# Optimization experiments

Hardware: AMD Instinct MI355X
Metric: run time of the kernel (lower is better)

## Reference

```python
import jax, jax.numpy as jnp
import numpy as np

K = 3           # kernel_size
PAD = 1         # padding
HEADS = 6
C = 192
CH = C // HEADS           # channels per head = 32
SCALE = CH ** (-0.5)
KK = K * K                # 9


def unfold3(x):
    # x: [N,C,H,W] -> [N,C,9,H,W] (im2col with k=3, pad=1, stride=1)
    N, c, H, W = x.shape
    xp = jnp.pad(x, ((0, 0), (0, 0), (PAD, PAD), (PAD, PAD)))
    return jnp.stack([xp[:, :, i:i + H, j:j + W] for i in range(K) for j in range(K)], axis=2)


def fold3(y):
    # y: [N,C,9,H,W] -> [N,C,H,W] (scatter-add inverse of unfold3)
    N, c, kk, H, W = y.shape
    out = jnp.zeros((N, c, H + 2 * PAD, W + 2 * PAD), dtype=y.dtype)
    idx = 0
    for i in range(K):
        for j in range(K):
            out = out.at[:, :, i:i + H, j:j + W].add(y[:, :, idx])
            idx += 1
    return out[:, :, PAD:PAD + H, PAD:PAD + W]


def setup_inputs() -> dict:
    key = jax.random.key(0)
    ks = jax.random.split(key, 6)
    N, H, W = 16, 56, 56
    s = 0.02
    return {
        "x": jax.random.normal(ks[0], (N, C, H, W), jnp.float32),
        "Wv": jax.random.normal(ks[1], (C, C), jnp.float32) * s,          # fc (no bias)
        "Wa": jax.random.normal(ks[2], (C, KK * KK * HEADS), jnp.float32) * s,  # fc_att weight
        "ba": jax.random.normal(ks[3], (KK * KK * HEADS,), jnp.float32) * s,
        "Wp": jax.random.normal(ks[4], (C, C), jnp.float32) * s,          # fc_proj weight
        "bp": jax.random.normal(ks[5], (C,), jnp.float32) * s,
    }


def reference(x, Wv, Wa, ba, Wp, bp):
    N, c, H, W = x.shape
    HW = H * W
    # value projection (pointwise linear over channels)
    v = jnp.einsum("nchw,cd->ndhw", x, Wv)
    # unfold values: [N,C,9,H,W] -> [N,heads,ch,9,HW] -> [N,heads,HW,9,ch]
    vu = unfold3(v).reshape(N, HEADS, CH, KK, HW).transpose(0, 1, 4, 3, 2)
    # attention logits from (avg-pooled, here identity since stride=1) input
    att = jnp.einsum("nchw,ck->nhwk", x, Wa) + ba       # [N,H,W,81*heads]
    att = att.reshape(N, HW, HEADS, KK, KK).transpose(0, 2, 1, 3, 4)  # [N,heads,HW,9,9]
    att = jax.nn.softmax(att * SCALE, axis=-1)          # dropout is identity at inference
    # apply per-position 9x9 attention to the 9 gathered neighbors
    out = jnp.einsum("nhpkl,nhplc->nhpkc", att, vu)      # [N,heads,HW,9,ch]
    # fold back: layout (heads, ch, kk) matches unfold layout (C, kk)
    out = out.transpose(0, 1, 4, 3, 2).reshape(N, c, KK, H, W)
    folded = fold3(out)                                  # [N,C,H,W]
    # output projection
    return jnp.einsum("nchw,cd->ndhw", folded, Wp) + bp[None, :, None, None]
```

## Files before the change

### kernel.cpp

```cpp
#include <hip/hip_runtime.h>
#include <hip/hip_bf16.h>
#include <math.h>

#define HW 3136
#define NPOS 50176
#define NC 192
#define NHEADS 6
#define IMG 56
#define NATT 486
#define ATT_SCALE 0.17677669529663687f

typedef __attribute__((ext_vector_type(8))) short short8;
typedef __attribute__((ext_vector_type(8))) unsigned short ushort8;
typedef __attribute__((ext_vector_type(4))) float float4v;
typedef __attribute__((ext_vector_type(4))) unsigned int uint4v;

__device__ __forceinline__ float bf2f(unsigned short u) {
    unsigned int x = ((unsigned int)u) << 16;
    return __builtin_bit_cast(float, x);
}
__device__ __forceinline__ float bf2f_lo(unsigned int u) {
    return __builtin_bit_cast(float, u << 16);
}
__device__ __forceinline__ float bf2f_hi(unsigned int u) {
    return __builtin_bit_cast(float, u & 0xffff0000u);
}
__device__ __forceinline__ unsigned short f2bf(float f) {
    __hip_bfloat16 h = __float2bfloat16(f);
    return __builtin_bit_cast(unsigned short, h);
}
__device__ __forceinline__ void gload_lds16(const void* g, void* l) {
    __builtin_amdgcn_global_load_lds((const __attribute__((address_space(1))) void*)g,
                                     (__attribute__((address_space(3))) void*)l, 16, 0, 0);
}

__global__ __launch_bounds__(256) void transpose_x(const float* __restrict__ x,
                                                   unsigned short* __restrict__ xt)
{
    __shared__ float tile[64][65];
    int bx = blockIdx.x;
    int n = (bx * 64) / HW;
    int hw0 = (bx * 64) % HW;
    int c0 = blockIdx.y * 64;
    int tl = threadIdx.x & 63, tg = threadIdx.x >> 6;
    const float* xn = x + (size_t)n * NC * HW;
#pragma unroll
    for (int i = 0; i < 16; ++i)
        tile[tg * 16 + i][tl] = xn[(size_t)(c0 + tg * 16 + i) * HW + hw0 + tl];
    __syncthreads();
    unsigned short* xp = xt + ((size_t)n * HW + hw0) * NC + c0;
#pragma unroll
    for (int i = 0; i < 16; ++i) {
        int hwr = tg * 16 + i;
        xp[(size_t)hwr * NC + tl] = f2bf(tile[tl][hwr]);
    }
}

__global__ __launch_bounds__(256) void prep_weights(
    const float* __restrict__ Wv, const float* __restrict__ Wa, const float* __restrict__ Wp,
    const float* __restrict__ ba,
    unsigned short* __restrict__ Wall, unsigned short* __restrict__ Wpt,
    float* __restrict__ ball)
{
    int idx = blockIdx.x * 256 + threadIdx.x;
    if (idx < 36864) {
        int d = idx / 192, k = idx - d * 192;
        Wpt[idx] = f2bf(Wp[(size_t)k * NC + d]);
    }
    if (idx < 147456) {
        int d = idx / 192, k = idx - d * 192;
        unsigned short val;
        float bv = 0.f;
        if (d < 192) {
            val = f2bf(Wv[(size_t)k * NC + d]);
        } else {
            int dp = d - 192;
            int head = dp / 96, rr = dp - head * 96;
            int k9 = rr / 10, l = rr - k9 * 10;
            bool valid = (k9 < 9) && (l < 9);
            int src = head * 81 + k9 * 9 + l;
            val = valid ? f2bf(Wa[(size_t)k * NATT + src]) : (unsigned short)0;
            bv = valid ? ba[src] : 0.f;
        }
        Wall[idx] = val;
        if (k == 0) ball[d] = bv;
    }
}

__global__ __launch_bounds__(512, 4) void gemm_big(
    const unsigned short* __restrict__ A, const unsigned short* __restrict__ W,
    const float* __restrict__ ball,
    unsigned short* __restrict__ Vo, unsigned short* __restrict__ ATo)
{
    __shared__ __align__(16) unsigned short As[3][4096];
    __shared__ __align__(16) unsigned short Bs[3][4096];
    int t = threadIdx.x, lane = t & 63, wave = t >> 6;
    int bi = blockIdx.x;
    int slot = bi >> 3;
    int q6 = slot / 6;
    int rr_ = (bi & 7) + 8 * q6;
    int cc_ = slot - 6 * q6;
    int col0 = cc_ * 128, row0 = rr_ * 128;
    int fr = lane & 15, fq = lane >> 4;
    int wm = (wave >> 2) * 64, wn = (wave & 3) * 32;
    int srow = lane >> 2;
    int sg = ((lane & 3) ^ ((lane >> 3) & 3)) * 16;
    int rc = (fq ^ ((fr >> 1) & 3)) * 16;
    const char* Ab = (const char*)A;
    const char* Wb = (const char*)W;

    float4v acc[4][2] = {};

#define STAGE_BIG(buf, k0)                                                         \
    {                                                                              \
        gload_lds16(Ab + (size_t)(row0 + wave * 16 + srow) * 384 + (k0) * 2 + sg,  \
                    (char*)As[buf] + wave * 1024);                                 \
        gload_lds16(Wb + (size_t)(col0 + wave * 16 + srow) * 384 + (k0) * 2 + sg,  \
                    (char*)Bs[buf] + wave * 1024);                                 \
    }

    STAGE_BIG(0, 0);
    STAGE_BIG(1, 32);
#pragma unroll
    for (int s = 0; s < 6; ++s) {
        int buf = s % 3;
        if (s < 4) {
            STAGE_BIG((s + 2) % 3, (s + 2) * 32);
            asm volatile("s_waitcnt vmcnt(4)\n\ts_barrier" ::: "memory");
        } else if (s == 4) {
            asm volatile("s_waitcnt vmcnt(2)\n\ts_barrier" ::: "memory");
        } else {
            asm volatile("s_waitcnt vmcnt(0)\n\ts_barrier" ::: "memory");
        }
        short8 af[4], bf[2];
#pragma unroll
        for (int mi = 0; mi < 4; ++mi)
            af[mi] = *(const short8*)((const char*)As[buf] + (wm + mi * 16 + fr) * 64 + rc);
#pragma unroll
        for (int ni = 0; ni < 2; ++ni)
            bf[ni] = *(const short8*)((const char*)Bs[buf] + (wn + ni * 16 + fr) * 64 + rc);
        asm volatile("s_waitcnt lgkmcnt(0)\n\ts_barrier" ::: "memory");
#pragma unroll
        for (int mi = 0; mi < 4; ++mi)
#pragma unroll
            for (int ni = 0; ni < 2; ++ni)
                acc[mi][ni] = __builtin_amdgcn_mfma_f32_16x16x32_bf16(
                    af[mi], bf[ni], acc[mi][ni], 0, 0, 0);
    }

#pragma unroll
    for (int ni = 0; ni < 2; ++ni) {
        int col = col0 + wn + ni * 16 + fr;
        float b = ball[col];
        unsigned short* bptr;
        size_t rstr;
        bool valid;
        if (col < 192) {
            int hd = col >> 5, ch = col & 31;
            bptr = Vo + ((size_t)hd * NPOS) * 32 + ch;
            rstr = 32;
            valid = true;
        } else {
            int dp = col - 192;
            int hd = dp / 96, rr = dp - hd * 96;
            int k9 = rr / 10, l = rr - k9 * 10;
            valid = (k9 < 9);
            bptr = ATo + ((size_t)(hd * 9 + (k9 < 9 ? k9 : 8)) * NPOS) * 10 + l;
            rstr = 10;
        }
#pragma unroll
        for (int mi = 0; mi < 4; ++mi) {
            int row = row0 + wm + mi * 16 + fq * 4;
#pragma unroll
            for (int r = 0; r < 4; ++r) {
                unsigned short val = f2bf(acc[mi][ni][r] + b);
                if (valid) bptr[(size_t)(row + r) * rstr] = val;
            }
        }
    }
#undef STAGE_BIG
}

__global__ __launch_bounds__(256) void gemm_small(
    const unsigned short* __restrict__ A,
    const unsigned short* __restrict__ B,
    const float* __restrict__ bias, float* __restrict__ out)
{
    __shared__ __align__(16) unsigned short As[2][2048];
    __shared__ __align__(16) unsigned short Bs[2][8192];
    int t = threadIdx.x, lane = t & 63, wave = t >> 6;
    int n0 = blockIdx.x * 256, m0 = blockIdx.y * 64;
    int fr = lane & 15, fq = lane >> 4;
    int srow = lane >> 2;
    int sg = ((lane & 3) ^ ((lane >> 3) & 3)) * 16;
    int rc = (fq ^ ((fr >> 1) & 3)) * 16;
    const char* Ab = (const char*)A;
    const char* Bb = (const char*)B;

    float4v acc[4][4] = {};

#define STAGE_SMALL(buf, k0)                                                      \
    {                                                                             \
        gload_lds16(Ab + (size_t)(m0 + wave * 16 + srow) * 384 + (k0)*2 + sg,     \
                    (char*)As[buf] + wave * 1024);                                \
        _Pragma("unroll")                                                         \
        for (int i = 0; i < 4; ++i) {                                             \
            int j = wave * 4 + i;                                                 \
            gload_lds16(Bb + (size_t)(n0 + j * 16 + srow) * 384 + (k0)*2 + sg,    \
                        (char*)Bs[buf] + j * 1024);                               \
        }                                                                         \
    }

    STAGE_SMALL(0, 0);
    for (int s = 0; s < 6; ++s) {
        if (s < 5) {
            STAGE_SMALL((s + 1) & 1, (s + 1) * 32);
            asm volatile("s_waitcnt vmcnt(5)\n\ts_barrier" ::: "memory");
        } else {
            asm volatile("s_waitcnt vmcnt(0)\n\ts_barrier" ::: "memory");
        }
        int buf = s & 1;
        short8 af[4], bf[4];
#pragma unroll
        for (int mi = 0; mi < 4; ++mi)
            af[mi] = *(const short8*)((const char*)As[buf] + (mi * 16 + fr) * 64 + rc);
#pragma unroll
        for (int ni = 0; ni < 4; ++ni)
            bf[ni] = *(const short8*)((const char*)Bs[buf] + (wave * 64 + ni * 16 + fr) * 64 + rc);
        asm volatile("s_waitcnt lgkmcnt(0)\n\ts_barrier" ::: "memory");
#pragma unroll
        for (int mi = 0; mi < 4; ++mi)
#pragma unroll
            for (int ni = 0; ni < 4; ++ni)
                acc[mi][ni] = __builtin_amdgcn_mfma_f32_16x16x32_bf16(
                    af[mi], bf[ni], acc[mi][ni], 0, 0, 0);
    }

#pragma unroll
    for (int ni = 0; ni < 4; ++ni) {
        int n = n0 + wave * 64 + ni * 16 + fr;
        int img = n / HW, phw = n - img * HW;
        float* op = out + (size_t)img * (NC * HW) + phw;
#pragma unroll
        for (int mi = 0; mi < 4; ++mi) {
            int m = m0 + mi * 16 + fq * 4;
#pragma unroll
            for (int r = 0; r < 4; ++r)
                op[(size_t)(m + r) * HW] = acc[mi][ni][r] + bias[m + r];
        }
    }
#undef STAGE_SMALL
}

__global__ __launch_bounds__(256, 4) void fused_att_agg(
    const unsigned short* __restrict__ V, const unsigned short* __restrict__ AT,
    unsigned short* __restrict__ fold)
{
    __shared__ __align__(16) char vt[4 * 434 * 16];
    int t = threadIdx.x;
    int bid = blockIdx.x;
    int head = bid % NHEADS; int tmp = bid / NHEADS;
    int tcol = tmp & 1; tmp >>= 1;
    int trow = tmp % 7; int img = tmp / 7;
    int h0 = trow * 8, w0 = tcol * 28;

    const unsigned short* Vh = V + (size_t)head * NPOS * 32;
    ushort8 stg[6];
#pragma unroll
    for (int i = 0; i < 6; ++i) {
        int u = i * 256 + t;
        int slot = u >> 2, q = u & 3;
        int vrow = slot >> 5, vcol = slot & 31;
        int hh = h0 - 2 + vrow, ww = w0 - 2 + vcol;
        bool ok = (hh >= 0) & (hh < IMG) & (ww >= 0) & (ww < IMG);
        int hc = min(max(hh, 0), IMG - 1);
        int wcl = min(max(ww, 0), IMG - 1);
        ushort8 val = *(const ushort8*)(Vh + (size_t)(img * HW + hc * IMG + wcl) * 32 + q * 8);
        if (!ok) val = (ushort8){};
        stg[i] = val;
    }

    int ph = t / 28, pw = t - (t / 28) * 28;
    int h = h0 + ph, w = w0 + pw;
    float wc[25];
#pragma unroll
    for (int d = 0; d < 25; ++d) wc[d] = 0.f;
    if (t < 224) {
        int head9 = head * 9;
#pragma unroll
        for (int k = 0; k < 9; ++k) {
            const int oky = k / 3 - 1, okx = k % 3 - 1;
            int hh = h - oky, ww = w - okx;
            bool ok = (hh >= 0) & (hh < IMG) & (ww >= 0) & (ww < IMG);
            int hc = min(max(hh, 0), IMG - 1);
            int wcl = min(max(ww, 0), IMG - 1);
            size_t nidx = (size_t)img * HW + hc * IMG + wcl;
            const unsigned int* ap32 =
                (const unsigned int*)(AT + ((size_t)(head9 + k) * NPOS + nidx) * 10);
            unsigned int u0 = ap32[0], u1 = ap32[1], u2 = ap32[2], u3 = ap32[3], u4 = ap32[4];
            float a[9] = { bf2f_lo(u0), bf2f_hi(u0), bf2f_lo(u1), bf2f_hi(u1),
                           bf2f_lo(u2), bf2f_hi(u2), bf2f_lo(u3), bf2f_hi(u3),
                           bf2f_lo(u4) };
            float m = -1e30f;
#pragma unroll
            for (int l = 0; l < 9; ++l) m = fmaxf(m, a[l]);
            float s = 0.f;
#pragma unroll
            for (int l = 0; l < 9; ++l) {
                a[l] = __expf((a[l] - m) * ATT_SCALE);
                s += a[l];
            }
            float g = ok ? (1.f / s) : 0.f;
#pragma unroll
            for (int l = 0; l < 9; ++l) {
                const int dy = (l / 3 - 1) - oky + 2;
                const int dx = (l % 3 - 1) - okx + 2;
                wc[dy * 5 + dx] += a[l] * g;
            }
        }
    }

#pragma unroll
    for (int i = 0; i < 6; ++i) {
        int u = i * 256 + t;
        int slot = u >> 2, q = u & 3;
        int vrow = slot >> 5, vcol = slot & 31;
        *(ushort8*)(vt + q * (434 * 16) + (vrow * 36 + vcol) * 16) = stg[i];
    }
    __syncthreads();

    if (t < 224) {
        int base = (ph * 36 + pw) * 16;
        int pos = img * HW + h * IMG + w;
        unsigned short* fo = fold + (size_t)pos * NC + head * 32;
#pragma unroll
        for (int q = 0; q < 4; ++q) {
            const char* vq = vt + q * (434 * 16) + base;
            float acc[8];
#pragma unroll
            for (int j = 0; j < 8; ++j) acc[j] = 0.f;
#pragma unroll
            for (int d = 0; d < 25; ++d) {
                const int dy = d / 5, dx = d % 5;
                float wf = wc[d];
                uint4v vv = *(const uint4v*)(vq + (dy * 36 + dx) * 16);
#pragma unroll
                for (int z = 0; z < 4; ++z) {
                    acc[2 * z]     += wf * bf2f_lo(vv[z]);
                    acc[2 * z + 1] += wf * bf2f_hi(vv[z]);
                }
            }
            ushort8 ov;
#pragma unroll
            for (int j = 0; j < 8; ++j) ov[j] = f2bf(acc[j]);
            *(ushort8*)(fo + q * 8) = ov;
        }
    }
}

extern "C" void kernel_launch(void* const* d_in, const int* in_sizes, int n_in,
                              void* d_out, int out_size, void* d_ws, size_t ws_size,
                              hipStream_t stream)
{
    const float* x  = (const float*)d_in[0];
    const float* Wv = (const float*)d_in[1];
    const float* Wa = (const float*)d_in[2];
    const float* ba = (const float*)d_in[3];
    const float* Wp = (const float*)d_in[4];
    const float* bp = (const float*)d_in[5];
    float* out = (float*)d_out;

    unsigned short* xt   = (unsigned short*)d_ws;
    unsigned short* V    = xt + 9633792;
    unsigned short* AT   = V + 9633792;
    unsigned short* Wall = AT + 27095040;
    unsigned short* Wpt  = Wall + 147456;
    float*          ball = (float*)(Wpt + 36864);
    unsigned short* foldb = xt;

    dim3 blk(256);
    prep_weights<<<576, blk, 0, stream>>>(Wv, Wa, Wp, ba, Wall, Wpt, ball);
    transpose_x<<<dim3(784, 3), blk, 0, stream>>>(x, xt);
    gemm_big<<<2352, dim3(512), 0, stream>>>(xt, Wall, ball, V, AT);
    fused_att_agg<<<1344, blk, 0, stream>>>(V, AT, foldb);
    gemm_small<<<dim3(196, 3), blk, 0, stream>>>(Wpt, foldb, bp, out);
}
```

Measured before the change: 182.9 us.

## Vectorize gemm_big epilogue stores, retile gemm_small, hoist attention loads

gemm_big swaps its MFMA operands so each lane holds four consecutive output columns, which lets the epilogue write packed bf16 pairs (8-byte and 4-byte stores) instead of scattered 2-byte stores, with special cases for the 10-wide attention rows. gemm_small moves to 128-column tiles on a 1D grid with a grouped tile order, halving LDS use and adding a 4-blocks-per-CU launch bound to raise occupancy. fused_att_agg issues all attention-logit loads into registers before the LDS staging and barrier, then runs the softmax afterwards, so load latency overlaps with the staging. The packed attention stores depend on tricky column-alignment logic, and holding the raw logits across the barrier raises register pressure.

```diff
diff --git a/kernel.cpp b/kernel.cpp
--- a/kernel.cpp
+++ b/kernel.cpp
@@ -14,6 +14,7 @@
 typedef __attribute__((ext_vector_type(8))) unsigned short ushort8;
 typedef __attribute__((ext_vector_type(4))) float float4v;
 typedef __attribute__((ext_vector_type(4))) unsigned int uint4v;
+typedef __attribute__((ext_vector_type(2))) unsigned int uint2v;
 
 __device__ __forceinline__ float bf2f(unsigned short u) {
     unsigned int x = ((unsigned int)u) << 16;
@@ -28,6 +29,9 @@
 __device__ __forceinline__ unsigned short f2bf(float f) {
     __hip_bfloat16 h = __float2bfloat16(f);
     return __builtin_bit_cast(unsigned short, h);
+}
+__device__ __forceinline__ unsigned int pack2bf(float a, float b) {
+    return (unsigned int)f2bf(a) | ((unsigned int)f2bf(b) << 16);
 }
 __device__ __forceinline__ void gload_lds16(const void* g, void* l) {
     __builtin_amdgcn_global_load_lds((const __attribute__((address_space(1))) void*)g,
@@ -145,51 +149,71 @@
 #pragma unroll
             for (int ni = 0; ni < 2; ++ni)
                 acc[mi][ni] = __builtin_amdgcn_mfma_f32_16x16x32_bf16(
-                    af[mi], bf[ni], acc[mi][ni], 0, 0, 0);
+                    bf[ni], af[mi], acc[mi][ni], 0, 0, 0);
     }
 
 #pragma unroll
     for (int ni = 0; ni < 2; ++ni) {
-        int col = col0 + wn + ni * 16 + fr;
-        float b = ball[col];
-        unsigned short* bptr;
-        size_t rstr;
-        bool valid;
-        if (col < 192) {
-            int hd = col >> 5, ch = col & 31;
-            bptr = Vo + ((size_t)hd * NPOS) * 32 + ch;
-            rstr = 32;
-            valid = true;
+        int cb = col0 + wn + ni * 16 + fq * 4;
+        float4v bb = *(const float4v*)(ball + cb);
+        if (cb < 192) {
+            int hd = cb >> 5, ch = cb & 31;
+            unsigned short* vp = Vo + (size_t)hd * NPOS * 32 + ch;
+#pragma unroll
+            for (int mi = 0; mi < 4; ++mi) {
+                int pos = row0 + wm + mi * 16 + fr;
+                uint2v pk;
+                pk[0] = pack2bf(acc[mi][ni][0] + bb[0], acc[mi][ni][1] + bb[1]);
+                pk[1] = pack2bf(acc[mi][ni][2] + bb[2], acc[mi][ni][3] + bb[3]);
+                *(uint2v*)(vp + (size_t)pos * 32) = pk;
+            }
         } else {
-            int dp = col - 192;
-            int hd = dp / 96, rr = dp - hd * 96;
-            int k9 = rr / 10, l = rr - k9 * 10;
-            valid = (k9 < 9);
-            bptr = ATo + ((size_t)(hd * 9 + (k9 < 9 ? k9 : 8)) * NPOS) * 10 + l;
-            rstr = 10;
-        }
-#pragma unroll
-        for (int mi = 0; mi < 4; ++mi) {
-            int row = row0 + wm + mi * 16 + fq * 4;
-#pragma unroll
-            for (int r = 0; r < 4; ++r) {
-                unsigned short val = f2bf(acc[mi][ni][r] + b);
-                if (valid) bptr[(size_t)(row + r) * rstr] = val;
+            int dp = cb - 192;
+            int hd = dp / 96, rr2 = dp - hd * 96;
+            int k9 = rr2 / 10, l = rr2 - k9 * 10;
+            if (k9 < 9) {
+                unsigned short* rp  = ATo + ((size_t)(hd * 9 + k9) * NPOS) * 10 + l;
+                unsigned short* rp2 = ATo + ((size_t)(hd * 9 + k9 + 1) * NPOS) * 10;
+                bool full = (l <= 4);
+                bool c6 = (l == 6);
+                bool nx = (k9 + 1 < 9);
+#pragma unroll
+                for (int mi = 0; mi < 4; ++mi) {
+                    int pos = row0 + wm + mi * 16 + fr;
+                    unsigned short* q = rp + (size_t)pos * 10;
+                    unsigned int lo = pack2bf(acc[mi][ni][0] + bb[0], acc[mi][ni][1] + bb[1]);
+                    unsigned int hi = pack2bf(acc[mi][ni][2] + bb[2], acc[mi][ni][3] + bb[3]);
+                    if (full) {
+                        ((unsigned int*)q)[0] = lo;
+                        ((unsigned int*)q)[1] = hi;
+                    } else if (c6) {
+                        ((unsigned int*)q)[0] = lo;
+                        q[2] = f2bf(acc[mi][ni][2] + bb[2]);
+                    } else {
+                        q[0] = f2bf(acc[mi][ni][0] + bb[0]);
+                        if (nx) *(unsigned int*)(rp2 + (size_t)pos * 10) = hi;
+                    }
+                }
             }
         }
     }
 #undef STAGE_BIG
 }
 
-__global__ __launch_bounds__(256) void gemm_small(
+__global__ __launch_bounds__(256, 4) void gemm_small(
     const unsigned short* __restrict__ A,
     const unsigned short* __restrict__ B,
     const float* __restrict__ bias, float* __restrict__ out)
 {
     __shared__ __align__(16) unsigned short As[2][2048];
-    __shared__ __align__(16) unsigned short Bs[2][8192];
+    __shared__ __align__(16) unsigned short Bs[2][4096];
     int t = threadIdx.x, lane = t & 63, wave = t >> 6;
-    int n0 = blockIdx.x * 256, m0 = blockIdx.y * 64;
+    int bi = blockIdx.x;
+    int slot = bi >> 3;
+    int q3 = slot / 3;
+    int ntile = (bi & 7) + 8 * q3;
+    int mtile = slot - 3 * q3;
+    int n0 = ntile * 128, m0 = mtile * 64;
     int fr = lane & 15, fq = lane >> 4;
     int srow = lane >> 2;
     int sg = ((lane & 3) ^ ((lane >> 3) & 3)) * 16;
@@ -197,48 +221,46 @@
     const char* Ab = (const char*)A;
     const char* Bb = (const char*)B;
 
-    float4v acc[4][4] = {};
-
-#define STAGE_SMALL(buf, k0)                                                      \
-    {                                                                             \
-        gload_lds16(Ab + (size_t)(m0 + wave * 16 + srow) * 384 + (k0)*2 + sg,     \
-                    (char*)As[buf] + wave * 1024);                                \
-        _Pragma("unroll")                                                         \
-        for (int i = 0; i < 4; ++i) {                                             \
-            int j = wave * 4 + i;                                                 \
-            gload_lds16(Bb + (size_t)(n0 + j * 16 + srow) * 384 + (k0)*2 + sg,    \
-                        (char*)Bs[buf] + j * 1024);                               \
-        }                                                                         \
+    float4v acc[4][2] = {};
+
+#define STAGE_SMALL(buf, k0)                                                       \
+    {                                                                              \
+        gload_lds16(Ab + (size_t)(m0 + wave * 16 + srow) * 384 + (k0)*2 + sg,      \
+                    (char*)As[buf] + wave * 1024);                                 \
+        gload_lds16(Bb + (size_t)(n0 + wave * 16 + srow) * 384 + (k0)*2 + sg,      \
+                    (char*)Bs[buf] + wave * 1024);                                 \
+        gload_lds16(Bb + (size_t)(n0 + 64 + wave * 16 + srow) * 384 + (k0)*2 + sg, \
+                    (char*)Bs[buf] + 4096 + wave * 1024);                          \
     }
 
     STAGE_SMALL(0, 0);
     for (int s = 0; s < 6; ++s) {
         if (s < 5) {
             STAGE_SMALL((s + 1) & 1, (s + 1) * 32);
-            asm volatile("s_waitcnt vmcnt(5)\n\ts_barrier" ::: "memory");
+            asm volatile("s_waitcnt vmcnt(3)\n\ts_barrier" ::: "memory");
         } else {
             asm volatile("s_waitcnt vmcnt(0)\n\ts_barrier" ::: "memory");
         }
         int buf = s & 1;
-        short8 af[4], bf[4];
+        short8 af[4], bf[2];
 #pragma unroll
         for (int mi = 0; mi < 4; ++mi)
             af[mi] = *(const short8*)((const char*)As[buf] + (mi * 16 + fr) * 64 + rc);
 #pragma unroll
-        for (int ni = 0; ni < 4; ++ni)
-            bf[ni] = *(const short8*)((const char*)Bs[buf] + (wave * 64 + ni * 16 + fr) * 64 + rc);
+        for (int ni = 0; ni < 2; ++ni)
+            bf[ni] = *(const short8*)((const char*)Bs[buf] + (wave * 32 + ni * 16 + fr) * 64 + rc);
         asm volatile("s_waitcnt lgkmcnt(0)\n\ts_barrier" ::: "memory");
 #pragma unroll
         for (int mi = 0; mi < 4; ++mi)
 #pragma unroll
-            for (int ni = 0; ni < 4; ++ni)
+            for (int ni = 0; ni < 2; ++ni)
                 acc[mi][ni] = __builtin_amdgcn_mfma_f32_16x16x32_bf16(
                     af[mi], bf[ni], acc[mi][ni], 0, 0, 0);
     }
 
 #pragma unroll
-    for (int ni = 0; ni < 4; ++ni) {
-        int n = n0 + wave * 64 + ni * 16 + fr;
+    for (int ni = 0; ni < 2; ++ni) {
+        int n = n0 + wave * 32 + ni * 16 + fr;
         int img = n / HW, phw = n - img * HW;
         float* op = out + (size_t)img * (NC * HW) + phw;
 #pragma unroll
@@ -282,25 +304,46 @@
 
     int ph = t / 28, pw = t - (t / 28) * 28;
     int h = h0 + ph, w = w0 + pw;
-    float wc[25];
-#pragma unroll
-    for (int d = 0; d < 25; ++d) wc[d] = 0.f;
+    unsigned int ub[9][5];
     if (t < 224) {
         int head9 = head * 9;
 #pragma unroll
         for (int k = 0; k < 9; ++k) {
             const int oky = k / 3 - 1, okx = k % 3 - 1;
             int hh = h - oky, ww = w - okx;
-            bool ok = (hh >= 0) & (hh < IMG) & (ww >= 0) & (ww < IMG);
             int hc = min(max(hh, 0), IMG - 1);
             int wcl = min(max(ww, 0), IMG - 1);
             size_t nidx = (size_t)img * HW + hc * IMG + wcl;
             const unsigned int* ap32 =
                 (const unsigned int*)(AT + ((size_t)(head9 + k) * NPOS + nidx) * 10);
-            unsigned int u0 = ap32[0], u1 = ap32[1], u2 = ap32[2], u3 = ap32[3], u4 = ap32[4];
-            float a[9] = { bf2f_lo(u0), bf2f_hi(u0), bf2f_lo(u1), bf2f_hi(u1),
-                           bf2f_lo(u2), bf2f_hi(u2), bf2f_lo(u3), bf2f_hi(u3),
-                           bf2f_lo(u4) };
+#pragma unroll
+            for (int z = 0; z < 5; ++z) ub[k][z] = ap32[z];
+        }
+    }
+
+#pragma unroll
+    for (int i = 0; i < 6; ++i) {
+        int u = i * 256 + t;
+        int slot = u >> 2, q = u & 3;
+        int vrow = slot >> 5, vcol = slot & 31;
+        *(ushort8*)(vt + q * (434 * 16) + (vrow * 36 + vcol) * 16) = stg[i];
+    }
+    __syncthreads();
+
+    float wc[25];
+#pragma unroll
+    for (int d = 0; d < 25; ++d) wc[d] = 0.f;
+    if (t < 224) {
+#pragma unroll
+        for (int k = 0; k < 9; ++k) {
+            const int oky = k / 3 - 1, okx = k % 3 - 1;
+            int hh = h - oky, ww = w - okx;
+            bool ok = (hh >= 0) & (hh < IMG) & (ww >= 0) & (ww < IMG);
+            float a[9] = { bf2f_lo(ub[k][0]), bf2f_hi(ub[k][0]),
+                           bf2f_lo(ub[k][1]), bf2f_hi(ub[k][1]),
+                           bf2f_lo(ub[k][2]), bf2f_hi(ub[k][2]),
+                           bf2f_lo(ub[k][3]), bf2f_hi(ub[k][3]),
+                           bf2f_lo(ub[k][4]) };
             float m = -1e30f;
 #pragma unroll
             for (int l = 0; l < 9; ++l) m = fmaxf(m, a[l]);
@@ -319,15 +362,6 @@
             }
         }
     }
-
-#pragma unroll
-    for (int i = 0; i < 6; ++i) {
-        int u = i * 256 + t;
-        int slot = u >> 2, q = u & 3;
-        int vrow = slot >> 5, vcol = slot & 31;
-        *(ushort8*)(vt + q * (434 * 16) + (vrow * 36 + vcol) * 16) = stg[i];
-    }
-    __syncthreads();
 
     if (t < 224) {
         int base = (ph * 36 + pw) * 16;
@@ -383,5 +417,5 @@
     transpose_x<<<dim3(784, 3), blk, 0, stream>>>(x, xt);
     gemm_big<<<2352, dim3(512), 0, stream>>>(xt, Wall, ball, V, AT);
     fused_att_agg<<<1344, blk, 0, stream>>>(V, AT, foldb);
-    gemm_small<<<dim3(196, 3), blk, 0, stream>>>(Wpt, foldb, bp, out);
-}
+    gemm_small<<<1176, blk, 0, stream>>>(Wpt, foldb, bp, out);
+}
```

New measurement: 170.9 us. 1.07x faster.
